# Kernel tuning notes

Measured on AMD Instinct MI355X. Metric: run time of the kernel, lower is better.

Reference implementation:

```python
import jax, jax.numpy as jnp
import numpy as np
from jax import lax

PAD0, PAD1 = 2, 2  # kernel_size=3 -> pad = (3//2+1, (3+1)//2) = (2, 2)


def make_blur_kernel():
    k = jnp.array([1.0, 3.0, 3.0, 1.0], dtype=jnp.float32)
    k2 = k[None, :] * k[:, None]  # [4,4] binomial
    return k2 / jnp.sum(k2)


def setup_inputs() -> dict:
    key = jax.random.key(0)
    x = jax.random.normal(key, (16, 256, 128, 128), dtype=jnp.float32)
    kernel = make_blur_kernel()  # fixed (buffer) 4x4 normalized binomial filter
    return {"x": x, "kernel": kernel}


def reference(x, kernel):
    # upfirdn2d(x, k, up=1, down=1, padding=(2,2)):
    # zero-pad H and W by (2,2) each, depthwise FIR filter with the 4x4 kernel.
    # Kernel is symmetric, so correlation == convolution.
    C = x.shape[1]
    w = jnp.broadcast_to(kernel[None, None, :, :], (C, 1, 4, 4))  # depthwise OIHW
    out = lax.conv_general_dilated(
        x, w,
        window_strides=(1, 1),
        padding=((PAD0, PAD1), (PAD0, PAD1)),
        feature_group_count=C,
        dimension_numbers=("NCHW", "OIHW", "NCHW"),
    )
    # output: [16, 256, 129, 129] (H + pad0 + pad1 - 4 + 1)
    return out
```

## Files before the change

kernel.cpp:

```cpp
#include <hip/hip_runtime.h>


__global__ __launch_bounds__(512) void blur_half(
    const float* __restrict__ x,
    const float* __restrict__ kern,
    float* __restrict__ out)
{
    __shared__ __align__(16) float lds[68 * 128];

    const int tid  = threadIdx.x;
    const int bid  = blockIdx.x;
    const int img  = bid >> 1;
    const int s    = bid & 1;
    const int wv   = tid >> 6;
    const int lane = tid & 63;

    const float* __restrict__ xi = x + (size_t)img * (128 * 128);
    float* __restrict__ oi = out + (size_t)img * (129 * 129);

    const int P0 = s ? 0 : 1;
    const int P1 = s ? 32 : 33;
    for (int p = P0 + wv; p <= P1; p += 8) {
        const int row = 64 * s - 2 + 2 * p;
        const float* src = xi + (size_t)row * 128 + (lane << 2);
        const float* dst = &lds[p * 256];
        __builtin_amdgcn_global_load_lds(
            (const __attribute__((address_space(1))) unsigned int*)src,
            (__attribute__((address_space(3))) unsigned int*)dst, 16, 0, 0);
    }
    if (tid < 256) {
        if (s == 0) lds[tid] = 0.0f;
        else        lds[66 * 128 + tid] = 0.0f;
    }

    float w[4][4];
#pragma unroll
    for (int p = 0; p < 4; ++p)
#pragma unroll
        for (int q = 0; q < 4; ++q)
            w[p][q] = kern[4 * p + q];

    __syncthreads();

    const int c  = tid >> 5;
    const int g  = tid & 31;
    const bool lv = (g >= 1);

    float xv[4][8];

#define LLOAD(S, KK) do {                                                    \
        const float* pb_ = &lds[(4 * c + (KK)) * 128 + 4 * g - 4];           \
        float4 a_ = make_float4(0.f, 0.f, 0.f, 0.f);                         \
        if (lv) a_ = *(const float4*)pb_;                                    \
        float4 b_ = *(const float4*)(pb_ + 4);                               \
        xv[S][0] = a_.x; xv[S][1] = a_.y; xv[S][2] = a_.z; xv[S][3] = a_.w;  \
        xv[S][4] = b_.x; xv[S][5] = b_.y; xv[S][6] = b_.z; xv[S][7] = b_.w;  \
    } while (0)

#define ACCP(S, P) do {                                                      \
        o0 = fmaf(xv[S][0], w[P][0], o0);                                    \
        o1 = fmaf(xv[S][1], w[P][0], o1);                                    \
        o2 = fmaf(xv[S][2], w[P][0], o2);                                    \
        o3 = fmaf(xv[S][3], w[P][0], o3);                                    \
        o0 = fmaf(xv[S][1], w[P][1], o0);                                    \
        o1 = fmaf(xv[S][2], w[P][1], o1);                                    \
        o2 = fmaf(xv[S][3], w[P][1], o2);                                    \
        o3 = fmaf(xv[S][4], w[P][1], o3);                                    \
        o0 = fmaf(xv[S][2], w[P][2], o0);                                    \
        o1 = fmaf(xv[S][3], w[P][2], o1);                                    \
        o2 = fmaf(xv[S][4], w[P][2], o2);                                    \
        o3 = fmaf(xv[S][5], w[P][2], o3);                                    \
        o0 = fmaf(xv[S][3], w[P][3], o0);                                    \
        o1 = fmaf(xv[S][4], w[P][3], o1);                                    \
        o2 = fmaf(xv[S][5], w[P][3], o2);                                    \
        o3 = fmaf(xv[S][6], w[P][3], o3);                                    \
    } while (0)

#define CS(SA, SB, SC, SD, PO) do {                                          \
        float o0 = 0.f, o1 = 0.f, o2 = 0.f, o3 = 0.f;                        \
        ACCP(SA, 0); ACCP(SB, 1); ACCP(SC, 2); ACCP(SD, 3);                  \
        if (lv) { (PO)[0] = o0; (PO)[1] = o1; }                              \
        (PO)[2] = o2;                                                        \
        (PO)[3] = o3;                                                        \
    } while (0)

#define XROW(S, P) do {                                                      \
        e0 = fmaf(xv[S][4], w[P][0], e0);                                    \
        e0 = fmaf(xv[S][5], w[P][1], e0);                                    \
        e0 = fmaf(xv[S][6], w[P][2], e0);                                    \
        e0 = fmaf(xv[S][7], w[P][3], e0);                                    \
        e1 = fmaf(xv[S][5], w[P][0], e1);                                    \
        e1 = fmaf(xv[S][6], w[P][1], e1);                                    \
        e1 = fmaf(xv[S][7], w[P][2], e1);                                    \
        e2 = fmaf(xv[S][6], w[P][0], e2);                                    \
        e2 = fmaf(xv[S][7], w[P][1], e2);                                    \
    } while (0)

#define CSX(SA, SB, SC, SD, PO) do {                                         \
        if (g == 31) {                                                       \
            float e0 = 0.f, e1 = 0.f, e2 = 0.f;                              \
            XROW(SA, 0); XROW(SB, 1); XROW(SC, 2); XROW(SD, 3);              \
            (PO)[4] = e0; (PO)[5] = e1; (PO)[6] = e2;     \
        }                                                                    \
    } while (0)

    {
        float* po = oi + (size_t)(64 * s + 4 * c) * 129 + 4 * g - 2;
        LLOAD(0, 0); LLOAD(1, 1); LLOAD(2, 2); LLOAD(3, 3);
        CS(0, 1, 2, 3, po); CSX(0, 1, 2, 3, po); LLOAD(0, 4); po += 129;
        CS(1, 2, 3, 0, po); CSX(1, 2, 3, 0, po); LLOAD(1, 5); po += 129;
        CS(2, 3, 0, 1, po); CSX(2, 3, 0, 1, po); LLOAD(2, 6); po += 129;
        CS(3, 0, 1, 2, po); CSX(3, 0, 1, 2, po); po += 129;
        if (s == 1 && c == 15) {
            LLOAD(3, 7);
            CS(0, 1, 2, 3, po); CSX(0, 1, 2, 3, po);
        }
    }

#undef LLOAD
#undef ACCP
#undef CS
#undef XROW
#undef CSX
}

extern "C" void kernel_launch(void* const* d_in, const int* in_sizes, int n_in,
                              void* d_out, int out_size, void* d_ws, size_t ws_size,
                              hipStream_t stream) {
    const float* x    = (const float*)d_in[0];
    const float* kern = (const float*)d_in[1];
    float* out        = (float*)d_out;

    dim3 grid(8192), block(512);
    hipLaunchKernelGGL(blur_half, grid, block, 0, stream, x, kern, out);
}
```

Measured before the change: 112.2 us.

## Remap block order, branchless left-halo loads, move right-edge columns to dedicated threads

Block IDs are permuted so that consecutive blocks map to images 1024 apart, changing how work is spread across XCDs and caches. The left-halo load now reads from a zeroed LDS row instead of taking a predicated branch. The right-edge output columns, which were computed by lane g==31 in every row iteration, are now computed by a separate group of 64-65 threads that read straight from LDS. This removes divergent tail work from the main loop, at the cost of an extra serialized phase for those threads and a slightly larger LDS buffer.

```diff
diff --git a/kernel.cpp b/kernel.cpp
--- a/kernel.cpp
+++ b/kernel.cpp
@@ -1,17 +1,18 @@
 #include <hip/hip_runtime.h>
 
 
-__global__ __launch_bounds__(512) void blur_half(
+__global__ __launch_bounds__(512) void blur_half2(
     const float* __restrict__ x,
     const float* __restrict__ kern,
     float* __restrict__ out)
 {
-    __shared__ __align__(16) float lds[68 * 128];
+    __shared__ __align__(16) float lds[69 * 128];
 
     const int tid  = threadIdx.x;
     const int bid  = blockIdx.x;
-    const int img  = bid >> 1;
-    const int s    = bid & 1;
+    const int wk   = ((bid & 7) << 10) | (bid >> 3);
+    const int img  = wk >> 1;
+    const int s    = wk & 1;
     const int wv   = tid >> 6;
     const int lane = tid & 63;
 
@@ -29,8 +30,10 @@
             (__attribute__((address_space(3))) unsigned int*)dst, 16, 0, 0);
     }
     if (tid < 256) {
-        if (s == 0) lds[tid] = 0.0f;
-        else        lds[66 * 128 + tid] = 0.0f;
+        if (s) lds[8448 + tid] = 0.0f;
+        else   lds[tid]        = 0.0f;
+    } else if (tid < 384) {
+        lds[8448 + tid] = 0.0f;
     }
 
     float w[4][4];
@@ -45,14 +48,15 @@
     const int c  = tid >> 5;
     const int g  = tid & 31;
     const bool lv = (g >= 1);
+    const float* const zrow = &lds[68 * 128];
 
     float xv[4][8];
 
 #define LLOAD(S, KK) do {                                                    \
-        const float* pb_ = &lds[(4 * c + (KK)) * 128 + 4 * g - 4];           \
-        float4 a_ = make_float4(0.f, 0.f, 0.f, 0.f);                         \
-        if (lv) a_ = *(const float4*)pb_;                                    \
-        float4 b_ = *(const float4*)(pb_ + 4);                               \
+        const float* pb_ = &lds[(4 * c + (KK)) * 128 + 4 * g];               \
+        const float* pa_ = lv ? (pb_ - 4) : zrow;                            \
+        float4 a_ = *(const float4*)pa_;                                     \
+        float4 b_ = *(const float4*)pb_;                                     \
         xv[S][0] = a_.x; xv[S][1] = a_.y; xv[S][2] = a_.z; xv[S][3] = a_.w;  \
         xv[S][4] = b_.x; xv[S][5] = b_.y; xv[S][6] = b_.z; xv[S][7] = b_.w;  \
     } while (0)
@@ -84,44 +88,41 @@
         (PO)[3] = o3;                                                        \
     } while (0)
 
-#define XROW(S, P) do {                                                      \
-        e0 = fmaf(xv[S][4], w[P][0], e0);                                    \
-        e0 = fmaf(xv[S][5], w[P][1], e0);                                    \
-        e0 = fmaf(xv[S][6], w[P][2], e0);                                    \
-        e0 = fmaf(xv[S][7], w[P][3], e0);                                    \
-        e1 = fmaf(xv[S][5], w[P][0], e1);                                    \
-        e1 = fmaf(xv[S][6], w[P][1], e1);                                    \
-        e1 = fmaf(xv[S][7], w[P][2], e1);                                    \
-        e2 = fmaf(xv[S][6], w[P][0], e2);                                    \
-        e2 = fmaf(xv[S][7], w[P][1], e2);                                    \
-    } while (0)
-
-#define CSX(SA, SB, SC, SD, PO) do {                                         \
-        if (g == 31) {                                                       \
-            float e0 = 0.f, e1 = 0.f, e2 = 0.f;                              \
-            XROW(SA, 0); XROW(SB, 1); XROW(SC, 2); XROW(SD, 3);              \
-            (PO)[4] = e0; (PO)[5] = e1; (PO)[6] = e2;     \
-        }                                                                    \
-    } while (0)
-
     {
         float* po = oi + (size_t)(64 * s + 4 * c) * 129 + 4 * g - 2;
         LLOAD(0, 0); LLOAD(1, 1); LLOAD(2, 2); LLOAD(3, 3);
-        CS(0, 1, 2, 3, po); CSX(0, 1, 2, 3, po); LLOAD(0, 4); po += 129;
-        CS(1, 2, 3, 0, po); CSX(1, 2, 3, 0, po); LLOAD(1, 5); po += 129;
-        CS(2, 3, 0, 1, po); CSX(2, 3, 0, 1, po); LLOAD(2, 6); po += 129;
-        CS(3, 0, 1, 2, po); CSX(3, 0, 1, 2, po); po += 129;
+        CS(0, 1, 2, 3, po); LLOAD(0, 4); po += 129;
+        CS(1, 2, 3, 0, po); LLOAD(1, 5); po += 129;
+        CS(2, 3, 0, 1, po); LLOAD(2, 6); po += 129;
+        CS(3, 0, 1, 2, po); po += 129;
         if (s == 1 && c == 15) {
             LLOAD(3, 7);
-            CS(0, 1, 2, 3, po); CSX(0, 1, 2, 3, po);
+            CS(0, 1, 2, 3, po);
         }
+    }
+
+    if (tid < (unsigned)(64 + s)) {
+        float e0 = 0.f, e1 = 0.f, e2 = 0.f;
+#pragma unroll
+        for (int p = 0; p < 4; ++p) {
+            float4 v = *(const float4*)&lds[(tid + p) * 128 + 124];
+            e0 = fmaf(v.x, w[p][0], e0);
+            e0 = fmaf(v.y, w[p][1], e0);
+            e0 = fmaf(v.z, w[p][2], e0);
+            e0 = fmaf(v.w, w[p][3], e0);
+            e1 = fmaf(v.y, w[p][0], e1);
+            e1 = fmaf(v.z, w[p][1], e1);
+            e1 = fmaf(v.w, w[p][2], e1);
+            e2 = fmaf(v.z, w[p][0], e2);
+            e2 = fmaf(v.w, w[p][1], e2);
+        }
+        float* po = oi + (size_t)(64 * s + tid) * 129 + 126;
+        po[0] = e0; po[1] = e1; po[2] = e2;
     }
 
 #undef LLOAD
 #undef ACCP
 #undef CS
-#undef XROW
-#undef CSX
 }
 
 extern "C" void kernel_launch(void* const* d_in, const int* in_sizes, int n_in,
@@ -132,5 +133,5 @@
     float* out        = (float*)d_out;
 
     dim3 grid(8192), block(512);
-    hipLaunchKernelGGL(blur_half, grid, block, 0, stream, x, kern, out);
+    hipLaunchKernelGGL(blur_half2, grid, block, 0, stream, x, kern, out);
 }
```

Result: slower. 114.8 us (+2.4%).

## Stage output rows through LDS for coalesced stores and remap block order

Applied to the files above, without the earlier changes.

Each half-wave now writes its 4-wide output results into a per-wave LDS buffer, then stores the 129-wide row with lane-contiguous scalar writes instead of strided unaligned writes. The misaligned row pitch of 129 had made direct stores poorly coalesced. Block IDs are also permuted across XCDs, and the left-edge predicated load is replaced by a pointer to a zeroed LDS row. The change costs extra LDS traffic and an lgkmcnt wait per row, and uses more shared memory.

```diff
diff --git a/kernel.cpp b/kernel.cpp
--- a/kernel.cpp
+++ b/kernel.cpp
@@ -1,17 +1,18 @@
 #include <hip/hip_runtime.h>
 
 
-__global__ __launch_bounds__(512) void blur_half(
+__global__ __launch_bounds__(512) void blur_half3(
     const float* __restrict__ x,
     const float* __restrict__ kern,
     float* __restrict__ out)
 {
-    __shared__ __align__(16) float lds[68 * 128];
+    __shared__ __align__(16) float lds[69 * 128 + 8 * 264];
 
     const int tid  = threadIdx.x;
     const int bid  = blockIdx.x;
-    const int img  = bid >> 1;
-    const int s    = bid & 1;
+    const int wk   = ((bid & 7) << 10) | (bid >> 3);
+    const int img  = wk >> 1;
+    const int s    = wk & 1;
     const int wv   = tid >> 6;
     const int lane = tid & 63;
 
@@ -29,8 +30,10 @@
             (__attribute__((address_space(3))) unsigned int*)dst, 16, 0, 0);
     }
     if (tid < 256) {
-        if (s == 0) lds[tid] = 0.0f;
-        else        lds[66 * 128 + tid] = 0.0f;
+        if (s) lds[8448 + tid] = 0.0f;
+        else   lds[tid]        = 0.0f;
+    } else if (tid < 384) {
+        lds[8448 + tid] = 0.0f;
     }
 
     float w[4][4];
@@ -45,14 +48,16 @@
     const int c  = tid >> 5;
     const int g  = tid & 31;
     const bool lv = (g >= 1);
+    const float* const zrow = &lds[68 * 128];
+    float* const obuf = &lds[69 * 128 + wv * 264 + (c & 1) * 132];
 
     float xv[4][8];
 
 #define LLOAD(S, KK) do {                                                    \
-        const float* pb_ = &lds[(4 * c + (KK)) * 128 + 4 * g - 4];           \
-        float4 a_ = make_float4(0.f, 0.f, 0.f, 0.f);                         \
-        if (lv) a_ = *(const float4*)pb_;                                    \
-        float4 b_ = *(const float4*)(pb_ + 4);                               \
+        const float* pb_ = &lds[(4 * c + (KK)) * 128 + 4 * g];               \
+        const float* pa_ = lv ? (pb_ - 4) : zrow;                            \
+        float4 a_ = *(const float4*)pa_;                                     \
+        float4 b_ = *(const float4*)pb_;                                     \
         xv[S][0] = a_.x; xv[S][1] = a_.y; xv[S][2] = a_.z; xv[S][3] = a_.w;  \
         xv[S][4] = b_.x; xv[S][5] = b_.y; xv[S][6] = b_.z; xv[S][7] = b_.w;  \
     } while (0)
@@ -76,14 +81,6 @@
         o3 = fmaf(xv[S][6], w[P][3], o3);                                    \
     } while (0)
 
-#define CS(SA, SB, SC, SD, PO) do {                                          \
-        float o0 = 0.f, o1 = 0.f, o2 = 0.f, o3 = 0.f;                        \
-        ACCP(SA, 0); ACCP(SB, 1); ACCP(SC, 2); ACCP(SD, 3);                  \
-        if (lv) { (PO)[0] = o0; (PO)[1] = o1; }                              \
-        (PO)[2] = o2;                                                        \
-        (PO)[3] = o3;                                                        \
-    } while (0)
-
 #define XROW(S, P) do {                                                      \
         e0 = fmaf(xv[S][4], w[P][0], e0);                                    \
         e0 = fmaf(xv[S][5], w[P][1], e0);                                    \
@@ -96,32 +93,43 @@
         e2 = fmaf(xv[S][7], w[P][1], e2);                                    \
     } while (0)
 
-#define CSX(SA, SB, SC, SD, PO) do {                                         \
+#define CS(SA, SB, SC, SD, J) do {                                           \
+        float o0 = 0.f, o1 = 0.f, o2 = 0.f, o3 = 0.f;                        \
+        ACCP(SA, 0); ACCP(SB, 1); ACCP(SC, 2); ACCP(SD, 3);                  \
+        *(float4*)&obuf[4 * g] = make_float4(o0, o1, o2, o3);                \
         if (g == 31) {                                                       \
             float e0 = 0.f, e1 = 0.f, e2 = 0.f;                              \
             XROW(SA, 0); XROW(SB, 1); XROW(SC, 2); XROW(SD, 3);              \
-            (PO)[4] = e0; (PO)[5] = e1; (PO)[6] = e2;     \
+            *(float2*)&obuf[128] = make_float2(e0, e1);    \
+            obuf[130] = e2;                                \
+        }                                                                    \
+        asm volatile("s_waitcnt lgkmcnt(0)" ::: "memory");                   \
+        __builtin_amdgcn_sched_barrier(0);                                   \
+        {                                                                    \
+            float* po_ = oi + (size_t)(64 * s + 4 * c + (J)) * 129;          \
+            _Pragma("unroll")                                                \
+            for (int k_ = 0; k_ < 4; ++k_)                                   \
+                po_[g + 32 * k_] = obuf[2 + g + 32 * k_];                    \
+            if (g == 0) po_[128] = obuf[130];                                \
         }                                                                    \
     } while (0)
 
     {
-        float* po = oi + (size_t)(64 * s + 4 * c) * 129 + 4 * g - 2;
         LLOAD(0, 0); LLOAD(1, 1); LLOAD(2, 2); LLOAD(3, 3);
-        CS(0, 1, 2, 3, po); CSX(0, 1, 2, 3, po); LLOAD(0, 4); po += 129;
-        CS(1, 2, 3, 0, po); CSX(1, 2, 3, 0, po); LLOAD(1, 5); po += 129;
-        CS(2, 3, 0, 1, po); CSX(2, 3, 0, 1, po); LLOAD(2, 6); po += 129;
-        CS(3, 0, 1, 2, po); CSX(3, 0, 1, 2, po); po += 129;
+        CS(0, 1, 2, 3, 0); LLOAD(0, 4);
+        CS(1, 2, 3, 0, 1); LLOAD(1, 5);
+        CS(2, 3, 0, 1, 2); LLOAD(2, 6);
+        CS(3, 0, 1, 2, 3);
         if (s == 1 && c == 15) {
             LLOAD(3, 7);
-            CS(0, 1, 2, 3, po); CSX(0, 1, 2, 3, po);
+            CS(0, 1, 2, 3, 4);
         }
     }
 
 #undef LLOAD
 #undef ACCP
+#undef XROW
 #undef CS
-#undef XROW
-#undef CSX
 }
 
 extern "C" void kernel_launch(void* const* d_in, const int* in_sizes, int n_in,
@@ -132,5 +140,5 @@
     float* out        = (float*)d_out;
 
     dim3 grid(8192), block(512);
-    hipLaunchKernelGGL(blur_half, grid, block, 0, stream, x, kern, out);
+    hipLaunchKernelGGL(blur_half3, grid, block, 0, stream, x, kern, out);
 }
```

After: 109.9 us (median of 2 runs). -2.1%, faster.

## Make blur kernel persistent with double-buffered async LDS staging of quarter-image tiles

Applied to the files above, without the earlier changes.

Replaces the one-block-per-half-image launch with 1024 persistent 256-thread blocks. Each block processes 16 quarter-image tiles, double-buffering async global-to-LDS loads so the next tile's fetch overlaps the current tile's compute. Border rows are handled by clamping load rows and redirecting reads to a shared zero row, not by zero-filling the buffer. This is meant to hide load latency and cut launch and tail overhead, at the cost of manual vmcnt waits, extra barriers and lower per-block parallelism.

```diff
diff --git a/kernel.cpp b/kernel.cpp
--- a/kernel.cpp
+++ b/kernel.cpp
@@ -1,58 +1,70 @@
 #include <hip/hip_runtime.h>
 
 
-__global__ __launch_bounds__(512) void blur_half(
+#define BAR() __builtin_amdgcn_s_barrier()
+#define WAITV(NSTR) do {                                                     \
+        asm volatile("s_waitcnt vmcnt(" NSTR ")" ::: "memory");              \
+        __builtin_amdgcn_sched_barrier(0);                                   \
+    } while (0)
+
+__global__ __launch_bounds__(256) void blur_persist(
     const float* __restrict__ x,
     const float* __restrict__ kern,
     float* __restrict__ out)
 {
-    __shared__ __align__(16) float lds[68 * 128];
+    __shared__ __align__(16) float lds[2 * 36 * 128 + 128];
 
     const int tid  = threadIdx.x;
-    const int bid  = blockIdx.x;
-    const int img  = bid >> 1;
-    const int s    = bid & 1;
     const int wv   = tid >> 6;
     const int lane = tid & 63;
+    const int c    = tid >> 5;
+    const int g    = tid & 31;
+    const bool lv  = (g >= 1);
 
-    const float* __restrict__ xi = x + (size_t)img * (128 * 128);
-    float* __restrict__ oi = out + (size_t)img * (129 * 129);
-
-    const int P0 = s ? 0 : 1;
-    const int P1 = s ? 32 : 33;
-    for (int p = P0 + wv; p <= P1; p += 8) {
-        const int row = 64 * s - 2 + 2 * p;
-        const float* src = xi + (size_t)row * 128 + (lane << 2);
-        const float* dst = &lds[p * 256];
-        __builtin_amdgcn_global_load_lds(
-            (const __attribute__((address_space(1))) unsigned int*)src,
-            (__attribute__((address_space(3))) unsigned int*)dst, 16, 0, 0);
-    }
-    if (tid < 256) {
-        if (s == 0) lds[tid] = 0.0f;
-        else        lds[66 * 128 + tid] = 0.0f;
-    }
+    const int bid  = blockIdx.x;
+    const int base = ((bid & 7) * 128 + (bid >> 3)) * 16;
 
     float w[4][4];
 #pragma unroll
     for (int p = 0; p < 4; ++p)
 #pragma unroll
-        for (int q = 0; q < 4; ++q)
-            w[p][q] = kern[4 * p + q];
+        for (int d = 0; d < 4; ++d)
+            w[p][d] = kern[4 * p + d];
 
-    __syncthreads();
+    if (tid < 128) lds[9216 + tid] = 0.0f;
+    asm volatile("s_waitcnt lgkmcnt(0)" ::: "memory");
+    const float* const zrow = &lds[9216];
 
-    const int c  = tid >> 5;
-    const int g  = tid & 31;
-    const bool lv = (g >= 1);
+#define STAGEPAIR(SB, XI, SS, PP) do {                                       \
+        int rr_ = 32 * (SS) - 2 + 2 * (PP);                                  \
+        rr_ = rr_ < 0 ? 0 : (rr_ > 126 ? 126 : rr_);      \
+        const float* src_ = (XI) + (size_t)rr_ * 128 + (lane << 2);          \
+        const float* dst_ = (SB) + (PP) * 256;                               \
+        __builtin_amdgcn_global_load_lds(                                    \
+            (const __attribute__((address_space(1))) unsigned int*)src_,     \
+            (__attribute__((address_space(3))) unsigned int*)dst_,           \
+            16, 0, 0);                                                       \
+    } while (0)
 
-    float xv[4][8];
+#define STAGE(TT) do {                                                       \
+        const int t_ = (TT);                                                 \
+        const int s_ = t_ & 3;                                               \
+        const float* xi_ = x + (size_t)(t_ >> 2) * 16384;                    \
+        float* sb_ = &lds[(t_ & 1) * 4608];                                  \
+        STAGEPAIR(sb_, xi_, s_, wv + 0);                                     \
+        STAGEPAIR(sb_, xi_, s_, wv + 4);                                     \
+        STAGEPAIR(sb_, xi_, s_, wv + 8);                                     \
+        STAGEPAIR(sb_, xi_, s_, wv + 12);                                    \
+        if (wv < 2) STAGEPAIR(sb_, xi_, s_, wv + 16);                        \
+    } while (0)
 
 #define LLOAD(S, KK) do {                                                    \
-        const float* pb_ = &lds[(4 * c + (KK)) * 128 + 4 * g - 4];           \
-        float4 a_ = make_float4(0.f, 0.f, 0.f, 0.f);                         \
-        if (lv) a_ = *(const float4*)pb_;                                    \
-        float4 b_ = *(const float4*)(pb_ + 4);                               \
+        const float* pb_ = sb + (4 * c + (KK)) * 128 + 4 * g;                \
+        const bool okr_ = (unsigned)(32 * s_ - 2 + 4 * c + (KK)) < 128u;     \
+        const float* pav_ = (okr_ && lv) ? (pb_ - 4) : zrow;                 \
+        const float* pbv_ = okr_ ? pb_ : zrow;                               \
+        float4 a_ = *(const float4*)pav_;                                    \
+        float4 b_ = *(const float4*)pbv_;                                    \
         xv[S][0] = a_.x; xv[S][1] = a_.y; xv[S][2] = a_.z; xv[S][3] = a_.w;  \
         xv[S][4] = b_.x; xv[S][5] = b_.y; xv[S][6] = b_.z; xv[S][7] = b_.w;  \
     } while (0)
@@ -76,14 +88,6 @@
         o3 = fmaf(xv[S][6], w[P][3], o3);                                    \
     } while (0)
 
-#define CS(SA, SB, SC, SD, PO) do {                                          \
-        float o0 = 0.f, o1 = 0.f, o2 = 0.f, o3 = 0.f;                        \
-        ACCP(SA, 0); ACCP(SB, 1); ACCP(SC, 2); ACCP(SD, 3);                  \
-        if (lv) { (PO)[0] = o0; (PO)[1] = o1; }                              \
-        (PO)[2] = o2;                                                        \
-        (PO)[3] = o3;                                                        \
-    } while (0)
-
 #define XROW(S, P) do {                                                      \
         e0 = fmaf(xv[S][4], w[P][0], e0);                                    \
         e0 = fmaf(xv[S][5], w[P][1], e0);                                    \
@@ -96,32 +100,54 @@
         e2 = fmaf(xv[S][7], w[P][1], e2);                                    \
     } while (0)
 
-#define CSX(SA, SB, SC, SD, PO) do {                                         \
+#define CS(SA, SB_, SC, SD, PO) do {                                         \
+        float o0 = 0.f, o1 = 0.f, o2 = 0.f, o3 = 0.f;                        \
+        ACCP(SA, 0); ACCP(SB_, 1); ACCP(SC, 2); ACCP(SD, 3);                 \
+        if (lv) { (PO)[0] = o0; (PO)[1] = o1; }                              \
+        (PO)[2] = o2;                                                        \
+        (PO)[3] = o3;                                                        \
         if (g == 31) {                                                       \
             float e0 = 0.f, e1 = 0.f, e2 = 0.f;                              \
-            XROW(SA, 0); XROW(SB, 1); XROW(SC, 2); XROW(SD, 3);              \
+            XROW(SA, 0); XROW(SB_, 1); XROW(SC, 2); XROW(SD, 3);             \
             (PO)[4] = e0; (PO)[5] = e1; (PO)[6] = e2;     \
         }                                                                    \
     } while (0)
 
-    {
-        float* po = oi + (size_t)(64 * s + 4 * c) * 129 + 4 * g - 2;
-        LLOAD(0, 0); LLOAD(1, 1); LLOAD(2, 2); LLOAD(3, 3);
-        CS(0, 1, 2, 3, po); CSX(0, 1, 2, 3, po); LLOAD(0, 4); po += 129;
-        CS(1, 2, 3, 0, po); CSX(1, 2, 3, 0, po); LLOAD(1, 5); po += 129;
-        CS(2, 3, 0, 1, po); CSX(2, 3, 0, 1, po); LLOAD(2, 6); po += 129;
-        CS(3, 0, 1, 2, po); CSX(3, 0, 1, 2, po); po += 129;
-        if (s == 1 && c == 15) {
-            LLOAD(3, 7);
-            CS(0, 1, 2, 3, po); CSX(0, 1, 2, 3, po);
-        }
+#define COMPUTE(TT) do {                                                     \
+        const int t_ = (TT);                                                 \
+        const int s_ = t_ & 3;                                               \
+        const float* sb = &lds[(t_ & 1) * 4608];                             \
+        float* oi_ = out + (size_t)(t_ >> 2) * 16641;                        \
+        float xv[4][8];                                                      \
+        float* po = oi_ + (size_t)(32 * s_ + 4 * c) * 129 + 4 * g - 2;       \
+        LLOAD(0, 0); LLOAD(1, 1); LLOAD(2, 2); LLOAD(3, 3);                  \
+        CS(0, 1, 2, 3, po); LLOAD(0, 4); po += 129;                          \
+        CS(1, 2, 3, 0, po); LLOAD(1, 5); po += 129;                          \
+        CS(2, 3, 0, 1, po); LLOAD(2, 6); po += 129;                          \
+        CS(3, 0, 1, 2, po); po += 129;                                       \
+        if (s_ == 3 && c == 7) {                  \
+            LLOAD(3, 7);                                                     \
+            CS(0, 1, 2, 3, po);                                              \
+        }                                                                    \
+    } while (0)
+
+    STAGE(base + 0);
+    STAGE(base + 1);
+    for (int i = 0; i < 16; ++i) {
+        if (wv < 2) WAITV("5"); else WAITV("4");
+        BAR();
+        COMPUTE(base + i);
+        BAR();
+        if (i < 14) STAGE(base + i + 2);
     }
 
+#undef STAGEPAIR
+#undef STAGE
 #undef LLOAD
 #undef ACCP
+#undef XROW
 #undef CS
-#undef XROW
-#undef CSX
+#undef COMPUTE
 }
 
 extern "C" void kernel_launch(void* const* d_in, const int* in_sizes, int n_in,
@@ -131,6 +157,6 @@
     const float* kern = (const float*)d_in[1];
     float* out        = (float*)d_out;
 
-    dim3 grid(8192), block(512);
-    hipLaunchKernelGGL(blur_half, grid, block, 0, stream, x, kern, out);
+    dim3 grid(1024), block(256);
+    hipLaunchKernelGGL(blur_persist, grid, block, 0, stream, x, kern, out);
 }
```

Result: slower. 138.5 us (+23.4%).
